# Optimization experiments

Hardware: AMD Instinct MI355X
Metric: run time of the kernel (lower is better)

The kernel has to match this reference:

```python
import jax, jax.numpy as jnp
import numpy as np

B, L, C = 512, 2048, 32  # batch, seq_len, num_labels


def setup_inputs() -> dict:
    key = jax.random.key(0)
    k1, k2, k3 = jax.random.split(key, 3)
    emissions = jax.random.normal(k1, (B, L, C), dtype=jnp.float32)
    tags = jax.random.randint(k2, (B, L), 0, C, dtype=jnp.int32)
    mask = jnp.ones((B, L), dtype=jnp.int32)
    # learned parameter: transitions (num_labels, num_labels)
    transitions = jax.random.normal(k3, (C, C), dtype=jnp.float32)
    return {"emissions": emissions, "transitions": transitions, "tags": tags, "mask": mask}


def _crf_nll(emissions, transitions, tags, mask):
    Bn, Ln, Cn = emissions.shape
    maskf = mask.astype(emissions.dtype)

    # ---- gold-path score (vectorized over the t loop) ----
    # emit[b,t] = emissions[b,t,tags[b,t]] for t in [0, L-2]
    emit = jnp.take_along_axis(emissions[:, : Ln - 1], tags[:, : Ln - 1, None], axis=2)[..., 0]
    # trans[b,t] = transitions[tags[b,t], tags[b,t+1]]
    trans = transitions[tags[:, : Ln - 1], tags[:, 1:]]
    score = jnp.sum(emit * maskf[:, : Ln - 1] + trans * maskf[:, 1:], axis=1)

    msum = jnp.sum(mask, axis=1)
    last_idx = jnp.clip(msum - 1, 0)  # index of last valid tag
    last_tag = jnp.take_along_axis(tags, last_idx[:, None], axis=1)[:, 0]
    le_t = jnp.clip(msum, 1) - 1
    last_emission = emissions[jnp.arange(Bn), le_t, last_tag]
    score = score + last_emission

    # ---- log-partition via forward algorithm (lax.scan over time) ----
    # Faithful to source: alpha_t[b,n,p] = alpha[b,p] + transitions[n,p] + emit[b,n],
    # reduced over p; the source's mask line is an algebraic no-op (a*m + a*(1-m) = a).
    def step(alpha, emit_t):
        # alpha: (B, C) over prev label p; emit_t: (B, C) over next label n
        alpha_new = jax.nn.logsumexp(alpha[:, None, :] + transitions[None, :, :], axis=2) + emit_t
        return alpha_new, None

    alpha0 = emissions[:, 0]                      # (B, C)
    em_rest = jnp.swapaxes(emissions[:, 1:], 0, 1)  # (L-1, B, C)
    alpha, _ = jax.lax.scan(step, alpha0, em_rest)
    log_Z = jax.nn.logsumexp(alpha, axis=1)       # (B,)

    return jnp.mean(log_Z - score)


def reference(emissions, transitions, tags, mask):
    return _crf_nll(emissions, transitions, tags, mask)
```

## Files before the change

kernel.cpp:

```cpp
#include <hip/hip_runtime.h>
#include <stdint.h>

typedef short bf16x8 __attribute__((ext_vector_type(8)));
typedef float f32x16 __attribute__((ext_vector_type(16)));

#define LN2f  0.69314718055994530942f

constexpr int Bn = 512;
constexpr int Ln = 2048;
constexpr int Cn = 32;
constexpr int NSEG = 64;
constexpr int SEGLEN = 32;
constexpr int WARM = 16;
constexpr int NGRP = 16;
constexpr int WPB  = 4;
constexpr int DEPTH = 8;

__device__ __forceinline__ uint32_t pack2_bf16(float lo, float hi) {
    uint32_t a = __float_as_uint(lo) + 0x8000u;
    uint32_t b = __float_as_uint(hi) + 0x8000u;
    return __builtin_amdgcn_perm(b, a, 0x07060302u);
}

__device__ __forceinline__ void gload16(const float* g, float* l) {
    __builtin_amdgcn_global_load_lds(
        (__attribute__((address_space(1))) void*)g,
        (__attribute__((address_space(3))) void*)l,
        16, 0, 0);
}

__global__ __launch_bounds__(256, 1) void crf_scan(
    const float* __restrict__ emis, const float* __restrict__ trans,
    float* __restrict__ dDelta)
{
    __shared__ float ELDS[WPB][DEPTH][1024];
    const int lane = threadIdx.x & 63;
    const int wid  = threadIdx.x >> 6;
    const int h    = lane >> 5;
    const int bl   = lane & 31;
    const int bl7  = bl & 7;
    const int unit = blockIdx.x * WPB + wid;
    const int g    = unit & (NGRP - 1);
    const int s    = unit >> 4;
    const int b    = g * 32 + bl;

    uint32_t gqb[4];
    {
        const int lr = lane >> 3;
        const int lc = lane & 7;
        #pragma unroll
        for (int q = 0; q < 4; ++q) {
            int br = 8 * q + lr;
            int sg = lc ^ lr;
            gqb[q] = (uint32_t)((g * 32 + br) * (Ln * Cn) + sg * 4);
        }
    }

    bf16x8 A1, A2;
    {
        float e1[8], e2[8];
        #pragma unroll
        for (int j = 0; j < 8; ++j) {
            int c1 = 4 * h + (j & 3) + 8 * (j >> 2);
            e1[j] = __expf(trans[bl * Cn + c1]);
            e2[j] = __expf(trans[bl * Cn + c1 + 16]);
        }
        union { uint32_t u[4]; bf16x8 v; } ua, ub;
        #pragma unroll
        for (int q = 0; q < 4; ++q) {
            ua.u[q] = pack2_bf16(e1[2*q], e1[2*q+1]);
            ub.u[q] = pack2_bf16(e2[2*q], e2[2*q+1]);
        }
        A1 = ua.v; A2 = ub.v;
    }

    const f32x16 zeroC = {0.f,0.f,0.f,0.f,0.f,0.f,0.f,0.f,0.f,0.f,0.f,0.f,0.f,0.f,0.f,0.f};

    f32x16 Dv;
    bf16x8 B1, B2;
    float  Eg[2][16];
    float  offF = 0.f;

    const int t0 = (s == 0) ? 0 : s * SEGLEN - WARM;

    auto issueTile = [&](int t, int slot) {
        const float* gp = emis + (size_t)t * Cn;
        #pragma unroll
        for (int q = 0; q < 4; ++q)
            gload16(gp + gqb[q], &ELDS[wid][slot][q * 256]);
    };

    auto readRaw = [&](int slot, float4 (&bu)[4]) {
        #pragma unroll
        for (int q = 0; q < 4; ++q) {
            int c16 = (h + 2 * q) ^ bl7;
            bu[q] = *(const float4*)&ELDS[wid][slot][bl * 32 + c16 * 4];
        }
    };

    auto packB = [&]() {
        union { uint32_t u[4]; bf16x8 v; } p1, p2;
        #pragma unroll
        for (int q = 0; q < 4; ++q) {
            p1.u[q] = pack2_bf16(Dv[2*q],     Dv[2*q + 1]);
            p2.u[q] = pack2_bf16(Dv[8 + 2*q], Dv[8 + 2*q + 1]);
        }
        B1 = p1.v; B2 = p2.v;
    };

    auto sumD = [&]() {
        float t = 0.f;
        #pragma unroll
        for (int r = 0; r < 16; ++r) t += Dv[r];
        t += __shfl_xor(t, 32, 64);
        return t;
    };

    auto step = [&](int u, bool isInit, int mode, int tIssue) {
        asm volatile("s_waitcnt vmcnt(20)" ::: "memory");
        float4 bu[4];
        readRaw((u + 2) & 7, bu);
        const int par = u & 1;
        if (isInit) {
            #pragma unroll
            for (int r = 0; r < 16; ++r) Dv[r] = Eg[par][r];
        } else {
            f32x16 acc = __builtin_amdgcn_mfma_f32_32x32x16_bf16(A1, B1, zeroC, 0, 0, 0);
            acc = __builtin_amdgcn_mfma_f32_32x32x16_bf16(A2, B2, acc, 0, 0, 0);
            #pragma unroll
            for (int r = 0; r < 16; ++r) Dv[r] = acc[r] * Eg[par][r];
        }
        if (u == 7) {
            if (mode == 1) {
                float m0 = fmaxf(fmaxf(Dv[0], Dv[1]),  fmaxf(Dv[2],  Dv[3]));
                float m1 = fmaxf(fmaxf(Dv[4], Dv[5]),  fmaxf(Dv[6],  Dv[7]));
                float m2 = fmaxf(fmaxf(Dv[8], Dv[9]),  fmaxf(Dv[10], Dv[11]));
                float m3 = fmaxf(fmaxf(Dv[12],Dv[13]), fmaxf(Dv[14], Dv[15]));
                float m  = fmaxf(fmaxf(m0, m1), fmaxf(m2, m3));
                m = fmaxf(m, __shfl_xor(m, 32, 64));
                int k = (int)((__float_as_uint(m) >> 23) & 0xffu) - 126;
                offF += (float)k * LN2f;
                float sc = __uint_as_float((uint32_t)(127 - k) << 23);
                #pragma unroll
                for (int r = 0; r < 16; ++r) Dv[r] *= sc;
            } else if (mode == 2) {
                float S = sumD();
                float inv = 1.0f / S;
                offF = 0.f;
                #pragma unroll
                for (int r = 0; r < 16; ++r) Dv[r] *= inv;
            }
        }
        packB();
        #pragma unroll
        for (int q = 0; q < 4; ++q) {
            Eg[par][4*q+0] = __expf(bu[q].x);
            Eg[par][4*q+1] = __expf(bu[q].y);
            Eg[par][4*q+2] = __expf(bu[q].z);
            Eg[par][4*q+3] = __expf(bu[q].w);
        }
        asm volatile("" ::: "memory");
        issueTile(min(tIssue, Ln - 1), u);
    };

    #pragma unroll
    for (int i2 = 0; i2 < DEPTH; ++i2) issueTile(min(t0 + i2, Ln - 1), i2);
    asm volatile("s_waitcnt vmcnt(24)" ::: "memory");
    {
        float4 r0[4], r1[4];
        readRaw(0, r0);
        readRaw(1, r1);
        #pragma unroll
        for (int q = 0; q < 4; ++q) {
            Eg[0][4*q+0] = __expf(r0[q].x);  Eg[0][4*q+1] = __expf(r0[q].y);
            Eg[0][4*q+2] = __expf(r0[q].z);  Eg[0][4*q+3] = __expf(r0[q].w);
            Eg[1][4*q+0] = __expf(r1[q].x);  Eg[1][4*q+1] = __expf(r1[q].y);
            Eg[1][4*q+2] = __expf(r1[q].z);  Eg[1][4*q+3] = __expf(r1[q].w);
        }
    }

    if (s == 0) {
        step(0, true, 0, t0 + 8);
        #pragma unroll
        for (int u = 1; u < 8; ++u) step(u, false, (u == 7) ? 1 : 0, t0 + u + 8);
        #pragma unroll 1
        for (int blk = 1; blk < 4; ++blk) {
            const int base = blk * 8;
            #pragma unroll
            for (int u = 0; u < 8; ++u)
                step(u, false, (u == 7 && blk < 3) ? 1 : 0, t0 + base + u + 8);
        }
    } else {
        step(0, true, 0, t0 + 8);
        #pragma unroll
        for (int u = 1; u < 8; ++u) step(u, false, (u == 7) ? 1 : 0, t0 + u + 8);
        #pragma unroll
        for (int u = 0; u < 8; ++u) step(u, false, (u == 7) ? 2 : 0, t0 + 8 + u + 8);
        #pragma unroll 1
        for (int blk = 2; blk < 6; ++blk) {
            const int base = blk * 8;
            #pragma unroll
            for (int u = 0; u < 8; ++u)
                step(u, false, (u == 7 && blk < 5) ? 1 : 0, t0 + base + u + 8);
        }
    }

    float Sf = sumD();
    float delta = offF + __logf(Sf);
    if (lane < 32) {
        dDelta[s * Bn + b] = delta;
    }
}

__global__ __launch_bounds__(256) void crf_score(
    const float* __restrict__ emis, const float* __restrict__ trans,
    const int* __restrict__ tags, const int* __restrict__ mask,
    const float* __restrict__ dDelta, float* __restrict__ dVal)
{
    __shared__ float Tl[Cn * Cn];
    __shared__ float redS[4];
    __shared__ int   redM[4];
    const int b = blockIdx.x;
    const int tid = threadIdx.x;
    for (int i = tid; i < Cn * Cn; i += 256) Tl[i] = trans[i];
    __syncthreads();

    const size_t tB = (size_t)b * Ln;
    const size_t eb = (size_t)b * Ln * Cn;
    const int t0 = tid * 8;

    int tg[9], mk[9];
    {
        int4 a0 = *(const int4*)(tags + tB + t0);
        int4 a1 = *(const int4*)(tags + tB + t0 + 4);
        int4 c0 = *(const int4*)(mask + tB + t0);
        int4 c1 = *(const int4*)(mask + tB + t0 + 4);
        tg[0]=a0.x; tg[1]=a0.y; tg[2]=a0.z; tg[3]=a0.w;
        tg[4]=a1.x; tg[5]=a1.y; tg[6]=a1.z; tg[7]=a1.w;
        mk[0]=c0.x; mk[1]=c0.y; mk[2]=c0.z; mk[3]=c0.w;
        mk[4]=c1.x; mk[5]=c1.y; mk[6]=c1.z; mk[7]=c1.w;
        tg[8] = (t0 + 8 < Ln) ? tags[tB + t0 + 8] : 0;
        mk[8] = (t0 + 8 < Ln) ? mask[tB + t0 + 8] : 0;
    }

    float sc = 0.f; int ms = 0;
    #pragma unroll
    for (int u = 0; u < 8; ++u) {
        int t = t0 + u;
        ms += mk[u];
        if (t < Ln - 1) {
            sc += (float)mk[u]     * emis[eb + (size_t)t * Cn + tg[u]];
            sc += (float)mk[u + 1] * Tl[(tg[u] << 5) + tg[u + 1]];
        }
    }
    #pragma unroll
    for (int o = 32; o > 0; o >>= 1) {
        sc += __shfl_down(sc, o, 64);
        ms += __shfl_down(ms, o, 64);
    }
    if ((tid & 63) == 0) { redS[tid >> 6] = sc; redM[tid >> 6] = ms; }
    __syncthreads();

    if (tid < NSEG) {
        float lz = dDelta[(size_t)tid * Bn + b];
        #pragma unroll
        for (int o = 32; o > 0; o >>= 1) lz += __shfl_down(lz, o, 64);
        if (tid == 0) {
            float scT = redS[0] + redS[1] + redS[2] + redS[3];
            int   msT = redM[0] + redM[1] + redM[2] + redM[3];
            int last_idx = max(msT - 1, 0);
            int le_t     = max(msT, 1) - 1;
            int lt = tags[tB + last_idx];
            float le = emis[eb + (size_t)le_t * Cn + lt];
            dVal[b] = lz - (scT + le);
        }
    }
}

__global__ void crf_final(const float* __restrict__ dVal, float* __restrict__ out)
{
    __shared__ float red[8];
    int b = threadIdx.x;
    float val = dVal[b];
    #pragma unroll
    for (int o = 32; o > 0; o >>= 1) val += __shfl_down(val, o, 64);
    if ((b & 63) == 0) red[b >> 6] = val;
    __syncthreads();
    if (b == 0) {
        float t = 0.f;
        #pragma unroll
        for (int w = 0; w < 8; ++w) t += red[w];
        out[0] = t * (1.0f / (float)Bn);
    }
}

extern "C" void kernel_launch(void* const* d_in, const int* in_sizes, int n_in,
                              void* d_out, int out_size, void* d_ws, size_t ws_size,
                              hipStream_t stream)
{
    const float* emis  = (const float*)d_in[0];
    const float* trans = (const float*)d_in[1];
    const int*   tags  = (const int*)d_in[2];
    const int*   mask  = (const int*)d_in[3];
    float* wsf = (float*)d_ws;
    float* dDelta = wsf;
    float* dVal   = wsf + NSEG * Bn;
    crf_scan<<<(NGRP * NSEG) / WPB, 64 * WPB, 0, stream>>>(emis, trans, dDelta);
    crf_score<<<Bn, 256, 0, stream>>>(emis, trans, tags, mask, dDelta, dVal);
    crf_final<<<1, Bn, 0, stream>>>(dVal, (float*)d_out);
}
```

Before: 241.3 us.

## Replace direct global-to-LDS loads with register-staged prefetch and LDS ring

Swaps the global_load_lds async prefetch (8-deep LDS ring with explicit vmcnt waits) for ordinary global loads into registers. These are later written to a 4-slot LDS ring with a swizzled layout and read back as MFMA fragments. Prefetch distance is six timesteps, kept in a 4-entry register ring, and Eg becomes single-buffered. This drops the manual waitcnt handling and halves LDS use. It adds ds_write traffic, more VGPR pressure, and relies on compiler-inserted waits, which may stall the serial recurrence.

```diff
diff --git a/kernel.cpp b/kernel.cpp
--- a/kernel.cpp
+++ b/kernel.cpp
@@ -14,7 +14,7 @@
 constexpr int WARM = 16;
 constexpr int NGRP = 16;
 constexpr int WPB  = 4;
-constexpr int DEPTH = 8;
+constexpr int NSLOT = 4;
 
 __device__ __forceinline__ uint32_t pack2_bf16(float lo, float hi) {
     uint32_t a = __float_as_uint(lo) + 0x8000u;
@@ -22,39 +22,27 @@
     return __builtin_amdgcn_perm(b, a, 0x07060302u);
 }
 
-__device__ __forceinline__ void gload16(const float* g, float* l) {
-    __builtin_amdgcn_global_load_lds(
-        (__attribute__((address_space(1))) void*)g,
-        (__attribute__((address_space(3))) void*)l,
-        16, 0, 0);
-}
-
 __global__ __launch_bounds__(256, 1) void crf_scan(
     const float* __restrict__ emis, const float* __restrict__ trans,
     float* __restrict__ dDelta)
 {
-    __shared__ float ELDS[WPB][DEPTH][1024];
+    __shared__ float ELDS[WPB][NSLOT][1024];
     const int lane = threadIdx.x & 63;
     const int wid  = threadIdx.x >> 6;
     const int h    = lane >> 5;
     const int bl   = lane & 31;
     const int bl7  = bl & 7;
+    const int lr   = lane >> 3;
+    const int lc   = lane & 7;
     const int unit = blockIdx.x * WPB + wid;
     const int g    = unit & (NGRP - 1);
     const int s    = unit >> 4;
     const int b    = g * 32 + bl;
 
-    uint32_t gqb[4];
-    {
-        const int lr = lane >> 3;
-        const int lc = lane & 7;
-        #pragma unroll
-        for (int q = 0; q < 4; ++q) {
-            int br = 8 * q + lr;
-            int sg = lc ^ lr;
-            gqb[q] = (uint32_t)((g * 32 + br) * (Ln * Cn) + sg * 4);
-        }
-    }
+    uint32_t goff[4];
+    #pragma unroll
+    for (int q = 0; q < 4; ++q)
+        goff[q] = (uint32_t)((g * 32 + 8 * q + lr) * (Ln * Cn) + lc * 4);
 
     bf16x8 A1, A2;
     {
@@ -78,24 +66,29 @@
 
     f32x16 Dv;
     bf16x8 B1, B2;
-    float  Eg[2][16];
+    float  Eg[16];
+    float4 Rg[4][4];
     float  offF = 0.f;
 
     const int t0 = (s == 0) ? 0 : s * SEGLEN - WARM;
-
-    auto issueTile = [&](int t, int slot) {
-        const float* gp = emis + (size_t)t * Cn;
+    const int NT = (s == 0) ? SEGLEN : (SEGLEN + WARM);
+
+    auto gload = [&](int t, float4 (&dst)[4]) {
         #pragma unroll
         for (int q = 0; q < 4; ++q)
-            gload16(gp + gqb[q], &ELDS[wid][slot][q * 256]);
-    };
-
-    auto readRaw = [&](int slot, float4 (&bu)[4]) {
-        #pragma unroll
-        for (int q = 0; q < 4; ++q) {
-            int c16 = (h + 2 * q) ^ bl7;
-            bu[q] = *(const float4*)&ELDS[wid][slot][bl * 32 + c16 * 4];
-        }
+            dst[q] = *(const float4*)(emis + (size_t)goff[q] + (size_t)t * Cn);
+    };
+
+    auto dswrite = [&](int slot, const float4 (&src)[4]) {
+        #pragma unroll
+        for (int q = 0; q < 4; ++q)
+            *(float4*)&ELDS[wid][slot][(8 * q + lr) * 32 + (lc ^ lr) * 4] = src[q];
+    };
+
+    auto readFrag = [&](int slot, float4 (&bu)[4]) {
+        #pragma unroll
+        for (int q = 0; q < 4; ++q)
+            bu[q] = *(const float4*)&ELDS[wid][slot][bl * 32 + ((h + 2 * q) ^ bl7) * 4];
     };
 
     auto packB = [&]() {
@@ -116,92 +109,92 @@
         return t;
     };
 
-    auto step = [&](int u, bool isInit, int mode, int tIssue) {
-        asm volatile("s_waitcnt vmcnt(20)" ::: "memory");
+    auto step = [&](int u, int i, bool isInit, int mode) {
         float4 bu[4];
-        readRaw((u + 2) & 7, bu);
-        const int par = u & 1;
+        readFrag((u + 1) & 3, bu);
         if (isInit) {
             #pragma unroll
-            for (int r = 0; r < 16; ++r) Dv[r] = Eg[par][r];
+            for (int r = 0; r < 16; ++r) Dv[r] = Eg[r];
         } else {
             f32x16 acc = __builtin_amdgcn_mfma_f32_32x32x16_bf16(A1, B1, zeroC, 0, 0, 0);
             acc = __builtin_amdgcn_mfma_f32_32x32x16_bf16(A2, B2, acc, 0, 0, 0);
             #pragma unroll
-            for (int r = 0; r < 16; ++r) Dv[r] = acc[r] * Eg[par][r];
-        }
-        if (u == 7) {
-            if (mode == 1) {
-                float m0 = fmaxf(fmaxf(Dv[0], Dv[1]),  fmaxf(Dv[2],  Dv[3]));
-                float m1 = fmaxf(fmaxf(Dv[4], Dv[5]),  fmaxf(Dv[6],  Dv[7]));
-                float m2 = fmaxf(fmaxf(Dv[8], Dv[9]),  fmaxf(Dv[10], Dv[11]));
-                float m3 = fmaxf(fmaxf(Dv[12],Dv[13]), fmaxf(Dv[14], Dv[15]));
-                float m  = fmaxf(fmaxf(m0, m1), fmaxf(m2, m3));
-                m = fmaxf(m, __shfl_xor(m, 32, 64));
-                int k = (int)((__float_as_uint(m) >> 23) & 0xffu) - 126;
-                offF += (float)k * LN2f;
-                float sc = __uint_as_float((uint32_t)(127 - k) << 23);
-                #pragma unroll
-                for (int r = 0; r < 16; ++r) Dv[r] *= sc;
-            } else if (mode == 2) {
-                float S = sumD();
-                float inv = 1.0f / S;
-                offF = 0.f;
-                #pragma unroll
-                for (int r = 0; r < 16; ++r) Dv[r] *= inv;
-            }
+            for (int r = 0; r < 16; ++r) Dv[r] = acc[r] * Eg[r];
+        }
+        if (mode == 1) {
+            float m0 = fmaxf(fmaxf(Dv[0], Dv[1]),  fmaxf(Dv[2],  Dv[3]));
+            float m1 = fmaxf(fmaxf(Dv[4], Dv[5]),  fmaxf(Dv[6],  Dv[7]));
+            float m2 = fmaxf(fmaxf(Dv[8], Dv[9]),  fmaxf(Dv[10], Dv[11]));
+            float m3 = fmaxf(fmaxf(Dv[12],Dv[13]), fmaxf(Dv[14], Dv[15]));
+            float m  = fmaxf(fmaxf(m0, m1), fmaxf(m2, m3));
+            m = fmaxf(m, __shfl_xor(m, 32, 64));
+            int k = (int)((__float_as_uint(m) >> 23) & 0xffu) - 126;
+            offF += (float)k * LN2f;
+            float sc = __uint_as_float((uint32_t)(127 - k) << 23);
+            #pragma unroll
+            for (int r = 0; r < 16; ++r) Dv[r] *= sc;
+        } else if (mode == 2) {
+            float S = sumD();
+            float inv = 1.0f / S;
+            offF = 0.f;
+            #pragma unroll
+            for (int r = 0; r < 16; ++r) Dv[r] *= inv;
         }
         packB();
         #pragma unroll
         for (int q = 0; q < 4; ++q) {
-            Eg[par][4*q+0] = __expf(bu[q].x);
-            Eg[par][4*q+1] = __expf(bu[q].y);
-            Eg[par][4*q+2] = __expf(bu[q].z);
-            Eg[par][4*q+3] = __expf(bu[q].w);
-        }
-        asm volatile("" ::: "memory");
-        issueTile(min(tIssue, Ln - 1), u);
-    };
-
-    #pragma unroll
-    for (int i2 = 0; i2 < DEPTH; ++i2) issueTile(min(t0 + i2, Ln - 1), i2);
-    asm volatile("s_waitcnt vmcnt(24)" ::: "memory");
+            Eg[4*q+0] = __expf(bu[q].x);
+            Eg[4*q+1] = __expf(bu[q].y);
+            Eg[4*q+2] = __expf(bu[q].z);
+            Eg[4*q+3] = __expf(bu[q].w);
+        }
+        dswrite((u + 3) & 3, Rg[(u + 3) & 3]);
+        int tt = t0 + min(i + 6, NT - 1);
+        gload(tt, Rg[(u + 6) & 3]);
+    };
+
+    gload(t0 + 0, Rg[0]);
+    gload(t0 + 1, Rg[1]);
+    gload(t0 + 2, Rg[2]);
+    dswrite(0, Rg[0]);
+    dswrite(1, Rg[1]);
+    dswrite(2, Rg[2]);
+    gload(t0 + 3, Rg[3]);
+    gload(t0 + 4, Rg[0]);
+    gload(t0 + 5, Rg[1]);
     {
-        float4 r0[4], r1[4];
-        readRaw(0, r0);
-        readRaw(1, r1);
+        float4 b0[4];
+        readFrag(0, b0);
         #pragma unroll
         for (int q = 0; q < 4; ++q) {
-            Eg[0][4*q+0] = __expf(r0[q].x);  Eg[0][4*q+1] = __expf(r0[q].y);
-            Eg[0][4*q+2] = __expf(r0[q].z);  Eg[0][4*q+3] = __expf(r0[q].w);
-            Eg[1][4*q+0] = __expf(r1[q].x);  Eg[1][4*q+1] = __expf(r1[q].y);
-            Eg[1][4*q+2] = __expf(r1[q].z);  Eg[1][4*q+3] = __expf(r1[q].w);
+            Eg[4*q+0] = __expf(b0[q].x);  Eg[4*q+1] = __expf(b0[q].y);
+            Eg[4*q+2] = __expf(b0[q].z);  Eg[4*q+3] = __expf(b0[q].w);
         }
     }
 
     if (s == 0) {
-        step(0, true, 0, t0 + 8);
-        #pragma unroll
-        for (int u = 1; u < 8; ++u) step(u, false, (u == 7) ? 1 : 0, t0 + u + 8);
+        step(0, 0, true, 0);
+        #pragma unroll
+        for (int u = 1; u < 8; ++u) step(u, u, false, (u == 7) ? 1 : 0);
         #pragma unroll 1
         for (int blk = 1; blk < 4; ++blk) {
             const int base = blk * 8;
             #pragma unroll
             for (int u = 0; u < 8; ++u)
-                step(u, false, (u == 7 && blk < 3) ? 1 : 0, t0 + base + u + 8);
+                step(u, base + u, false, (u == 7 && blk < 3) ? 1 : 0);
         }
     } else {
-        step(0, true, 0, t0 + 8);
-        #pragma unroll
-        for (int u = 1; u < 8; ++u) step(u, false, (u == 7) ? 1 : 0, t0 + u + 8);
-        #pragma unroll
-        for (int u = 0; u < 8; ++u) step(u, false, (u == 7) ? 2 : 0, t0 + 8 + u + 8);
+        step(0, 0, true, 0);
+        #pragma unroll
+        for (int u = 1; u < 8; ++u) step(u, u, false, (u == 7) ? 1 : 0);
+        #pragma unroll
+        for (int u = 0; u < 8; ++u) step(u, 8 + u, false, (u == 7) ? 2 : 0);
         #pragma unroll 1
         for (int blk = 2; blk < 6; ++blk) {
             const int base = blk * 8;
             #pragma unroll
             for (int u = 0; u < 8; ++u)
-                step(u, false, (u == 7 && blk < 5) ? 1 : 0, t0 + base + u + 8);
+                step(u, base + u, false, (u == 7 && blk < 5) ? 1 : 0);
         }
     }
 
```

Result: slower. 334.8 us (+38.7%).
